# Kernel optimization log

Hardware: AMD Instinct MI355X
Metric: run time of the kernel (lower is better)

The kernel has to match this reference:

```python
import jax, jax.numpy as jnp
import numpy as np
from jax import lax

T_ITERS = 6
LN_EPS = 1e-5

def layer_norm(x, g, b):
    mu = jnp.mean(x, axis=-1, keepdims=True)
    var = jnp.var(x, axis=-1, keepdims=True)
    return (x - mu) * lax.rsqrt(var + LN_EPS) * g + b

def setup_inputs() -> dict:
    key = jax.random.key(0)
    ks = jax.random.split(key, 12)
    B, C_in, S = 8, 128, 33
    hidden = 2 * C_in          # 256
    dim = 256                  # feat_dim
    N = 64
    w = lambda k, shp, s=0.02: (jax.random.normal(k, shp, jnp.float32) * s)
    return {
        "x": jax.random.normal(ks[0], (B, C_in, S, S, S), jnp.float32),
        "templates_init": jax.random.normal(ks[1], (1, N, dim), jnp.float32),
        "conv_w": w(ks[2], (hidden, C_in, 3, 3, 3)),
        "conv_b": jnp.zeros((hidden,), jnp.float32),
        "Wq": w(ks[3], (dim, dim)),
        "Wk": w(ks[4], (hidden, dim)),
        "Wv": w(ks[5], (hidden, dim)),
        "ln_in_g": jnp.ones((hidden,), jnp.float32), "ln_in_b": jnp.zeros((hidden,), jnp.float32),
        "ln_t_g": jnp.ones((dim,), jnp.float32),    "ln_t_b": jnp.zeros((dim,), jnp.float32),
        "ln_m_g": jnp.ones((dim,), jnp.float32),    "ln_m_b": jnp.zeros((dim,), jnp.float32),
        "W1": w(ks[6], (dim, 2 * dim)), "b1": jnp.zeros((2 * dim,), jnp.float32),
        "W2": w(ks[7], (2 * dim, dim)), "b2": jnp.zeros((dim,), jnp.float32),
    }

def reference(x, templates_init, conv_w, conv_b, Wq, Wk, Wv,
              ln_in_g, ln_in_b, ln_t_g, ln_t_b, ln_m_g, ln_m_b,
              W1, b1, W2, b2):
    # project: Conv3d stride 2, no padding, + ReLU
    h = lax.conv_general_dilated(x, conv_w, window_strides=(2, 2, 2),
                                 padding='VALID',
                                 dimension_numbers=('NCDHW', 'OIDHW', 'NCDHW'))
    h = jax.nn.relu(h + conv_b[None, :, None, None, None])
    B, C, X, Y, Z = h.shape
    dim = templates_init.shape[-1]
    N = templates_init.shape[1]
    scale = dim ** (-0.5)
    tokens = h.reshape(B, C, X * Y * Z).transpose(0, 2, 1)   # (B, L, hidden)
    tokens = layer_norm(tokens, ln_in_g, ln_in_b)
    k = tokens @ Wk                                           # (B, L, dim)
    v = tokens @ Wv                                           # (B, L, dim)
    templates = jnp.broadcast_to(templates_init, (B, N, dim))
    attn = None
    for _ in range(T_ITERS):
        t_prev = templates
        t = layer_norm(templates, ln_t_g, ln_t_b)
        q = (t @ Wq) * scale                                  # (B, N, dim)
        attn_logits = jnp.einsum('bnd,bld->bln', q, k)        # (B, L, N)
        attn = jax.nn.softmax(attn_logits, axis=-1)           # competitive over N
        attn = attn + 1e-8
        attn = attn / jnp.sum(attn, axis=-2, keepdims=True)   # renormalize over L
        templates = t_prev + jnp.einsum('bld,bln->bnd', v, attn)
        m = layer_norm(templates, ln_m_g, ln_m_b)
        templates = templates + (jax.nn.gelu(m @ W1 + b1, approximate=False) @ W2 + b2)
    templates_out = templates.transpose(0, 2, 1)              # (B, dim, N)
    attn_out = attn.transpose(0, 2, 1).reshape(B, N, X, Y, Z)
    return templates_out, attn_out
```

## Files before the change

### kernel.cpp

```cpp
#include <hip/hip_runtime.h>

typedef unsigned short u16;
typedef short s16x8 __attribute__((ext_vector_type(8)));
typedef float f32x4 __attribute__((ext_vector_type(4)));
typedef float f32x4u __attribute__((ext_vector_type(4), aligned(4)));
typedef unsigned short us4 __attribute__((ext_vector_type(4)));

__device__ __forceinline__ float bf2f(u16 v) {
    return __uint_as_float(((unsigned int)v) << 16);
}
__device__ __forceinline__ u16 f2bf(float f) {
    unsigned int u = __float_as_uint(f);
    u = u + 0x7FFFu + ((u >> 16) & 1u);
    return (u16)(u >> 16);
}
__device__ __forceinline__ f32x4 mfma16(s16x8 a, s16x8 b, f32x4 c) {
    return __builtin_amdgcn_mfma_f32_16x16x32_bf16(a, b, c, 0, 0, 0);
}
#define ZERO4 f32x4{0.f, 0.f, 0.f, 0.f}

__global__ void prepack_kernel(const float* __restrict__ conv_w, const float* __restrict__ Wk,
                               const float* __restrict__ Wv, const float* __restrict__ Wq,
                               const float* __restrict__ W1, const float* __restrict__ W2,
                               u16* __restrict__ Bp, u16* __restrict__ WkvP, u16* __restrict__ WqP,
                               u16* __restrict__ W1T, u16* __restrict__ W2T)
{
    int idx = blockIdx.x * 256 + threadIdx.x;
    if (idx < 294912) {
        int n = idx / 1152, g = idx - n * 1152;
        int ic = g / 9, r = g - ic * 9;
        const float* s = conv_w + n * 3456 + ic * 27 + r * 3;
        u16* d = Bp + n * 4608 + g * 4;
        d[0] = f2bf(s[0]); d[1] = f2bf(s[1]); d[2] = f2bf(s[2]); d[3] = 0;
    } else if (idx < 425984) {
        int i = idx - 294912;
        int n = i >> 8, c = i & 255;
        WkvP[i] = f2bf((n < 256) ? Wk[c * 256 + n] : Wv[c * 256 + (n - 256)]);
    } else if (idx < 491520) {
        int i = idx - 425984;
        int n = i >> 8, c = i & 255;
        WqP[i] = f2bf(Wq[c * 256 + n]);
    } else if (idx < 622592) {
        int i = idx - 491520;
        int h = i >> 8, c = i & 255;
        W1T[i] = f2bf(W1[c * 512 + h]);
    } else if (idx < 753664) {
        int i = idx - 622592;
        int dd = i >> 9, h = i & 511;
        W2T[i] = f2bf(W2[h * 256 + dd]);
    }
}

__global__ __launch_bounds__(512, 4) void conv_fused(
    const float* __restrict__ x, const u16* __restrict__ Bp, const float* __restrict__ conv_b,
    const float* __restrict__ ln_g, const float* __restrict__ ln_b, const u16* __restrict__ WkvP,
    u16* __restrict__ kbuf, u16* __restrict__ vT)
{
    __shared__ __align__(16) char smem[66816];
    u16* slab0  = (u16*)smem;
    u16* slab1  = (u16*)(smem + 31104);
    u16* tokbf  = (u16*)smem;
    float* lnred  = (float*)(smem + 62208);
    float* lnstat = (float*)(smem + 66304);

    int blk = blockIdx.x;
    int b = blk & 7, ox = (blk >> 5) & 15, oyb = (blk >> 3) & 3;
    int tid = threadIdx.x, wid = tid >> 6, lane = tid & 63;
    int quad = lane >> 4, l15 = lane & 15;
    int nbase = wid * 32;

    f32x4 acc[4][2];
    #pragma unroll
    for (int i = 0; i < 4; ++i)
        #pragma unroll
        for (int j = 0; j < 2; ++j) acc[i][j] = ZERO4;

    const u16* bprow0 = Bp + (nbase + l15) * 4608 + quad * 8;
    const u16* bprow1 = bprow0 + 16 * 4608;

    const float* xp[8]; int so8[8]; unsigned wmask = 0;
    #pragma unroll
    for (int u = 0; u < 8; ++u) {
        int s = tid + u * 512;
        so8[u] = -1; xp[u] = x;
        if (s < 3888) {
            int row = s / 9;
            int c = s - row * 9;
            int icl = row / 27;
            int rr = row - icl * 27;
            int ixl = rr / 9;
            int iyl = rr - ixl * 9;
            const float* xr = x + ((size_t)((b * 128 + icl) * 33) + (2 * ox + ixl)) * 1089
                              + (8 * oyb + iyl) * 33;
            if (c < 8) { xp[u] = xr + c * 4; wmask |= (1u << u); }
            else       { xp[u] = xr + 32; }
            so8[u] = row * 36 + c * 4;
        }
    }
    const size_t ICST = 16ull * 35937;

    f32x4u tv[8];
#define LOADX(ICC)                                                          \
    {                                                                       \
        _Pragma("unroll")                                                   \
        for (int u = 0; u < 8; ++u) {                                       \
            if (so8[u] >= 0) {                                              \
                const float* p = xp[u] + (size_t)(ICC) * ICST;              \
                if ((wmask >> u) & 1u) tv[u] = *(const f32x4u*)p;           \
                else                   tv[u] = f32x4u{p[0], 0.f, 0.f, 0.f}; \
            }                                                               \
        }                                                                   \
    }
#define STOREX(DST)                                                         \
    {                                                                       \
        _Pragma("unroll")                                                   \
        for (int u = 0; u < 8; ++u) {                                       \
            if (so8[u] >= 0) {                                              \
                us4 w;                                                      \
                w.x = f2bf(tv[u].x); w.y = f2bf(tv[u].y);                   \
                w.z = f2bf(tv[u].z); w.w = f2bf(tv[u].w);                   \
                *(us4*)((DST) + so8[u]) = w;                                \
            }                                                               \
        }                                                                   \
    }

    LOADX(0)
    STOREX(slab0)
    __syncthreads();

    for (int icc = 0; icc < 8; ++icc) {
        const u16* cur = (icc & 1) ? slab1 : slab0;
        u16* nxt = (icc & 1) ? slab0 : slab1;
        if (icc < 7) LOADX(icc + 1)

        const u16* bk0 = bprow0 + icc * 576;
        const u16* bk1 = bprow1 + icc * 576;
        s16x8 bbA[2], bbB[2];
        bbA[0] = *reinterpret_cast<const s16x8*>(bk0);
        bbA[1] = *reinterpret_cast<const s16x8*>(bk1);

#define CONV_STEP(CC, BREG)                                                     \
        {                                                                       \
            int g = (CC) * 8 + quad * 2;                                        \
            int i0 = g / 9, r9 = g - i0 * 9;                                    \
            int kx = r9 / 3, ky = r9 - kx * 3;                                  \
            int base0 = (i0 * 27 + kx * 9 + ky) * 36 + 2 * l15;                 \
            g += 1;                                                             \
            i0 = g / 9; r9 = g - i0 * 9; kx = r9 / 3; ky = r9 - kx * 3;         \
            int base1 = (i0 * 27 + kx * 9 + ky) * 36 + 2 * l15;                 \
            _Pragma("unroll")                                                   \
            for (int fm = 0; fm < 4; ++fm) {                                    \
                union { s16x8 v; ushort2 h[4]; } af;                            \
                const u16* sp0 = cur + base0 + fm * 72;                         \
                const u16* sp1 = cur + base1 + fm * 72;                         \
                af.h[0] = *(const ushort2*)(sp0);                               \
                af.h[1] = *(const ushort2*)(sp0 + 2);                           \
                af.h[2] = *(const ushort2*)(sp1);                               \
                af.h[3] = *(const ushort2*)(sp1 + 2);                           \
                acc[fm][0] = mfma16(af.v, (BREG)[0], acc[fm][0]);               \
                acc[fm][1] = mfma16(af.v, (BREG)[1], acc[fm][1]);               \
            }                                                                   \
        }

        #pragma unroll 1
        for (int c8 = 0; c8 < 18; c8 += 2) {
            bbB[0] = *reinterpret_cast<const s16x8*>(bk0 + (c8 + 1) * 32);
            bbB[1] = *reinterpret_cast<const s16x8*>(bk1 + (c8 + 1) * 32);
            CONV_STEP(c8, bbA)
            if (c8 + 2 < 18) {
                bbA[0] = *reinterpret_cast<const s16x8*>(bk0 + (c8 + 2) * 32);
                bbA[1] = *reinterpret_cast<const s16x8*>(bk1 + (c8 + 2) * 32);
            }
            CONV_STEP(c8 + 1, bbB)
        }
#undef CONV_STEP
        if (icc < 7) STOREX(nxt)
        __syncthreads();
    }
#undef LOADX
#undef STOREX

    #pragma unroll
    for (int fn = 0; fn < 2; ++fn) {
        float bias = conv_b[nbase + fn * 16 + l15];
        #pragma unroll
        for (int fm = 0; fm < 4; ++fm)
            #pragma unroll
            for (int r = 0; r < 4; ++r)
                acc[fm][fn][r] = fmaxf(acc[fm][fn][r] + bias, 0.f);
    }
    #pragma unroll
    for (int fm = 0; fm < 4; ++fm) {
        #pragma unroll
        for (int r = 0; r < 4; ++r) {
            float s = acc[fm][0][r] + acc[fm][1][r];
            float q2 = acc[fm][0][r] * acc[fm][0][r] + acc[fm][1][r] * acc[fm][1][r];
            #pragma unroll
            for (int msk = 1; msk <= 8; msk <<= 1) {
                s  += __shfl_xor(s, msk, 64);
                q2 += __shfl_xor(q2, msk, 64);
            }
            if (l15 == 0) {
                int mm = fm * 16 + quad * 4 + r;
                lnred[(wid * 64 + mm) * 2 + 0] = s;
                lnred[(wid * 64 + mm) * 2 + 1] = q2;
            }
        }
    }
    __syncthreads();
    if (tid < 64) {
        float s = 0, q2 = 0;
        #pragma unroll
        for (int w = 0; w < 8; ++w) { s += lnred[(w * 64 + tid) * 2]; q2 += lnred[(w * 64 + tid) * 2 + 1]; }
        float mu = s * (1.f / 256.f);
        float var = fmaxf(q2 * (1.f / 256.f) - mu * mu, 0.f);
        lnstat[tid * 2]     = mu;
        lnstat[tid * 2 + 1] = rsqrtf(var + 1e-5f);
    }
    __syncthreads();
    {
        float gam[2], bet[2];
        #pragma unroll
        for (int fn = 0; fn < 2; ++fn) {
            int n = nbase + fn * 16 + l15;
            gam[fn] = ln_g[n]; bet[fn] = ln_b[n];
        }
        #pragma unroll
        for (int fm = 0; fm < 4; ++fm)
            #pragma unroll
            for (int r = 0; r < 4; ++r) {
                int mm = fm * 16 + quad * 4 + r;
                float mu = lnstat[mm * 2], rs = lnstat[mm * 2 + 1];
                #pragma unroll
                for (int fn = 0; fn < 2; ++fn) {
                    int n = nbase + fn * 16 + l15;
                    tokbf[mm * 264 + n] = f2bf((acc[fm][fn][r] - mu) * rs * gam[fn] + bet[fn]);
                }
            }
    }
    __syncthreads();
    f32x4 kacc[4][4];
    #pragma unroll
    for (int i = 0; i < 4; ++i)
        #pragma unroll
        for (int j = 0; j < 4; ++j) kacc[i][j] = ZERO4;
    int n2 = wid * 64;
    const u16* wp = WkvP + (n2 + l15) * 256 + quad * 8;
    s16x8 wvA[4], wvB[4];
    #pragma unroll
    for (int fn = 0; fn < 4; ++fn) wvA[fn] = *reinterpret_cast<const s16x8*>(wp + fn * 4096);

#define KV_STEP(KK, WREG)                                                           \
    {                                                                               \
        s16x8 a2[4];                                                                \
        _Pragma("unroll")                                                           \
        for (int fm = 0; fm < 4; ++fm)                                              \
            a2[fm] = *reinterpret_cast<const s16x8*>(tokbf + (fm * 16 + l15) * 264  \
                                                     + (KK) * 32 + quad * 8);       \
        _Pragma("unroll")                                                           \
        for (int fn = 0; fn < 4; ++fn)                                              \
            _Pragma("unroll")                                                       \
            for (int fm = 0; fm < 4; ++fm)                                          \
                kacc[fm][fn] = mfma16(a2[fm], (WREG)[fn], kacc[fm][fn]);            \
    }

    #pragma unroll 1
    for (int kc = 0; kc < 8; kc += 2) {
        #pragma unroll
        for (int fn = 0; fn < 4; ++fn)
            wvB[fn] = *reinterpret_cast<const s16x8*>(wp + fn * 4096 + (kc + 1) * 32);
        KV_STEP(kc, wvA)
        if (kc + 2 < 8) {
            #pragma unroll
            for (int fn = 0; fn < 4; ++fn)
                wvA[fn] = *reinterpret_cast<const s16x8*>(wp + fn * 4096 + (kc + 2) * 32);
        }
        KV_STEP(kc + 1, wvB)
    }
#undef KV_STEP

    #pragma unroll
    for (int fm = 0; fm < 4; ++fm)
        #pragma unroll
        for (int r = 0; r < 4; ++r) {
            int l = (ox * 16 + oyb * 4 + fm) * 16 + quad * 4 + r;
            #pragma unroll
            for (int fn = 0; fn < 4; ++fn) {
                int n = n2 + fn * 16 + l15;
                u16 v = f2bf(kacc[fm][fn][r]);
                if (n < 256) kbuf[((b << 12) + l) * 256 + n] = v;
                else         vT[((b * 256 + (n - 256)) << 12) + l] = v;
            }
        }
}

__global__ __launch_bounds__(256) void kQ(
    const float* __restrict__ tinit, float* __restrict__ tpl,
    const float* __restrict__ ln_t_g, const float* __restrict__ ln_t_b,
    const u16* __restrict__ WqP, u16* __restrict__ qbuf, float* __restrict__ delta)
{
    __shared__ __align__(16) u16 mls[64 * 264];
    __shared__ float pls[64][4][2];
    __shared__ float stat[64][2];
    int b = blockIdx.x, tid = threadIdx.x;
    int m = tid >> 2, part = tid & 3;
    const float* tp = tinit + m * 256 + part * 64;
    float* tg = tpl + (b * 64 + m) * 256 + part * 64;
    float s = 0, q2 = 0;
    for (int i = 0; i < 64; ++i) {
        float v = tp[i];
        tg[i] = v;
        s += v; q2 += v * v;
    }
    pls[m][part][0] = s; pls[m][part][1] = q2;
    __syncthreads();
    if (tid < 64) {
        float ss = 0, qq = 0;
        #pragma unroll
        for (int p = 0; p < 4; ++p) { ss += pls[tid][p][0]; qq += pls[tid][p][1]; }
        float mu = ss * (1.f / 256.f);
        float var = fmaxf(qq * (1.f / 256.f) - mu * mu, 0.f);
        stat[tid][0] = mu; stat[tid][1] = rsqrtf(var + 1e-5f);
    }
    __syncthreads();
    {
        float mu = stat[m][0], rs = stat[m][1];
        for (int i = 0; i < 64; ++i) {
            int d = part * 64 + i;
            mls[m * 264 + d] = f2bf((tp[i] - mu) * rs * ln_t_g[d] + ln_t_b[d]);
        }
    }
    __syncthreads();
    int wid = tid >> 6, lane = tid & 63, quad = lane >> 4, l15 = lane & 15;
    f32x4 qa[4][4];
    #pragma unroll
    for (int i = 0; i < 4; ++i)
        #pragma unroll
        for (int j = 0; j < 4; ++j) qa[i][j] = ZERO4;
    #pragma unroll 1
    for (int kc = 0; kc < 8; ++kc) {
        s16x8 a[4];
        #pragma unroll
        for (int fm = 0; fm < 4; ++fm)
            a[fm] = *reinterpret_cast<const s16x8*>(mls + (fm * 16 + l15) * 264 + kc * 32 + quad * 8);
        #pragma unroll
        for (int fn = 0; fn < 4; ++fn) {
            s16x8 bv = *reinterpret_cast<const s16x8*>(WqP + (wid * 64 + fn * 16 + l15) * 256 + kc * 32 + quad * 8);
            #pragma unroll
            for (int fm = 0; fm < 4; ++fm)
                qa[fm][fn] = mfma16(a[fm], bv, qa[fm][fn]);
        }
    }
    #pragma unroll
    for (int fm = 0; fm < 4; ++fm)
        #pragma unroll
        for (int fn = 0; fn < 4; ++fn)
            #pragma unroll
            for (int r = 0; r < 4; ++r) {
                int mt = fm * 16 + quad * 4 + r;
                int d = wid * 64 + fn * 16 + l15;
                qbuf[(b * 64 + mt) * 256 + d] = f2bf(qa[fm][fn][r] * 0.0625f);
            }
    f32x4* dz = (f32x4*)(delta + b * 16384);
    for (int i = tid; i < 4096; i += 256) dz[i] = ZERO4;
}

__global__ __launch_bounds__(512, 2) void kA(
    const u16* __restrict__ qbuf, const u16* __restrict__ kbuf, const u16* __restrict__ vT,
    float* __restrict__ cs_part, float* __restrict__ delta, int last, u16* __restrict__ attnT)
{
    __shared__ __align__(16) u16 qls[64 * 264];
    __shared__ __align__(16) u16 atile[64 * 136];
    __shared__ float colsh[8][64];
    int b = blockIdx.x & 7, ltg = blockIdx.x >> 3;
    int tid = threadIdx.x, wid = tid >> 6, lane = tid & 63;
    int quad = lane >> 4, l15 = lane & 15;

    {
        int r = tid >> 3, c = (tid & 7) * 32;
        const u16* src = qbuf + b * 16384 + r * 256 + c;
        u16* dst = qls + r * 264 + c;
        #pragma unroll
        for (int j = 0; j < 4; ++j)
            *(int4*)(dst + j * 8) = *(const int4*)(src + j * 8);
    }
    int lrow = ltg * 128 + wid * 16;
    const u16* arow = kbuf + (size_t)((b << 12) + lrow + l15) * 256;
    s16x8 av[8];
    #pragma unroll
    for (int kc = 0; kc < 8; ++kc)
        av[kc] = *reinterpret_cast<const s16x8*>(arow + kc * 32 + quad * 8);
    const u16* vrow = vT + ((size_t)(b * 256 + wid * 32 + l15) << 12) + ltg * 128 + quad * 8;
    s16x8 bv2[2][4];
    #pragma unroll
    for (int fn = 0; fn < 2; ++fn)
        #pragma unroll
        for (int kc = 0; kc < 4; ++kc)
            bv2[fn][kc] = *reinterpret_cast<const s16x8*>(vrow + (fn << 16) + kc * 32);
    __syncthreads();
    f32x4 sa[4];
    #pragma unroll
    for (int fn = 0; fn < 4; ++fn) sa[fn] = ZERO4;
    #pragma unroll
    for (int kc = 0; kc < 8; ++kc) {
        #pragma unroll
        for (int fn = 0; fn < 4; ++fn) {
            s16x8 bv = *reinterpret_cast<const s16x8*>(qls + (fn * 16 + l15) * 264 + kc * 32 + quad * 8);
            sa[fn] = mfma16(av[kc], bv, sa[fn]);
        }
    }
    float colp[4] = {0.f, 0.f, 0.f, 0.f};
    #pragma unroll
    for (int r = 0; r < 4; ++r) {
        float mx = fmaxf(fmaxf(sa[0][r], sa[1][r]), fmaxf(sa[2][r], sa[3][r]));
        #pragma unroll
        for (int msk = 1; msk <= 8; msk <<= 1) mx = fmaxf(mx, __shfl_xor(mx, msk, 64));
        float e[4], sum = 0;
        #pragma unroll
        for (int fn = 0; fn < 4; ++fn) { e[fn] = __expf(sa[fn][r] - mx); sum += e[fn]; }
        #pragma unroll
        for (int msk = 1; msk <= 8; msk <<= 1) sum += __shfl_xor(sum, msk, 64);
        float inv = 1.f / sum;
        #pragma unroll
        for (int fn = 0; fn < 4; ++fn) {
            float p = e[fn] * inv + 1e-8f;
            colp[fn] += p;
            atile[(fn * 16 + l15) * 136 + wid * 16 + quad * 4 + r] = f2bf(p);
        }
    }
    #pragma unroll
    for (int fn = 0; fn < 4; ++fn) {
        float c = colp[fn];
        c += __shfl_xor(c, 16, 64);
        c += __shfl_xor(c, 32, 64);
        if (lane < 16) colsh[wid][fn * 16 + lane] = c;
    }
    __syncthreads();
    if (tid < 64) {
        float s = 0;
        #pragma unroll
        for (int w = 0; w < 8; ++w) s += colsh[w][tid];
        cs_part[((b << 5) + ltg) * 64 + tid] = s;
    }
    {
        f32x4 pacc[4][2];
        #pragma unroll
        for (int i = 0; i < 4; ++i)
            #pragma unroll
            for (int j = 0; j < 2; ++j) pacc[i][j] = ZERO4;
        #pragma unroll
        for (int kc = 0; kc < 4; ++kc) {
            #pragma unroll
            for (int fm = 0; fm < 4; ++fm) {
                s16x8 a = *reinterpret_cast<const s16x8*>(atile + (fm * 16 + l15) * 136 + kc * 32 + quad * 8);
                #pragma unroll
                for (int fn = 0; fn < 2; ++fn)
                    pacc[fm][fn] = mfma16(a, bv2[fn][kc], pacc[fm][fn]);
            }
        }
        #pragma unroll
        for (int fm = 0; fm < 4; ++fm)
            #pragma unroll
            for (int fn = 0; fn < 2; ++fn)
                #pragma unroll
                for (int r = 0; r < 4; ++r) {
                    int n = fm * 16 + quad * 4 + r;
                    int d = wid * 32 + fn * 16 + l15;
                    atomicAdd(&delta[(size_t)(b * 64 + n) * 256 + d], pacc[fm][fn][r]);
                }
    }
    if (last) {
        int n = tid >> 3, lo = (tid & 7) * 16;
        const u16* src = atile + n * 136 + lo;
        u16* dst = attnT + (size_t)((b * 64 + n) << 12) + ltg * 128 + lo;
        *(int4*)(dst)     = *(const int4*)(src);
        *(int4*)(dst + 8) = *(const int4*)(src + 8);
    }
}

__global__ __launch_bounds__(512) void kT(
    float* __restrict__ tpl, float* __restrict__ delta, const float* __restrict__ cs_part,
    float* __restrict__ colsum,
    const float* __restrict__ ln_m_g, const float* __restrict__ ln_m_b,
    const u16* __restrict__ W1T, const float* __restrict__ b1,
    const u16* __restrict__ W2T, const float* __restrict__ b2,
    const float* __restrict__ ln_t_g, const float* __restrict__ ln_t_b,
    const u16* __restrict__ WqP, u16* __restrict__ qbuf,
    int last, float* __restrict__ out0)
{
    __shared__ __align__(16) u16 mls[16 * 264];
    __shared__ __align__(16) u16 hid[16 * 520];
    __shared__ float pls[16][32][2];
    __shared__ float stat[16][2];
    __shared__ float lnr2[8][16][2];
    __shared__ float csh[16];
    int b = blockIdx.x & 7, mg = blockIdx.x >> 3;
    int m0 = mg * 16;
    int tid = threadIdx.x, wid = tid >> 6, lane = tid & 63;
    int quad = lane >> 4, l15 = lane & 15;
    if (tid < 16) {
        float s = 0;
        #pragma unroll
        for (int g = 0; g < 32; ++g) s += cs_part[((b << 5) + g) * 64 + m0 + tid];
        csh[tid] = 1.f / s;
        if (last) colsum[b * 64 + m0 + tid] = s;
    }
    __syncthreads();
    {
        int ml = tid >> 5, part = tid & 31;
        float cinv = csh[ml];
        float* tg = tpl + (b * 64 + m0 + ml) * 256 + part * 8;
        float* dg = delta + (size_t)(b * 64 + m0 + ml) * 256 + part * 8;
        float vbuf[8];
        float s = 0, q2 = 0;
        #pragma unroll
        for (int i = 0; i < 8; ++i) {
            float v = tg[i] + dg[i] * cinv;
            vbuf[i] = v; s += v; q2 += v * v;
        }
        if (!last) {
            f32x4* dz = (f32x4*)dg;
            dz[0] = ZERO4; dz[1] = ZERO4;
        }
        pls[ml][part][0] = s; pls[ml][part][1] = q2;
        __syncthreads();
        if (tid < 16) {
            float ss = 0, qq = 0;
            #pragma unroll
            for (int p = 0; p < 32; ++p) { ss += pls[tid][p][0]; qq += pls[tid][p][1]; }
            float mu = ss * (1.f / 256.f);
            float var = fmaxf(qq * (1.f / 256.f) - mu * mu, 0.f);
            stat[tid][0] = mu; stat[tid][1] = rsqrtf(var + 1e-5f);
        }
        __syncthreads();
        float mu = stat[ml][0], rs = stat[ml][1];
        #pragma unroll
        for (int i = 0; i < 8; ++i) {
            int d = part * 8 + i;
            tg[i] = vbuf[i];
            mls[ml * 264 + d] = f2bf((vbuf[i] - mu) * rs * ln_m_g[d] + ln_m_b[d]);
        }
    }
    __syncthreads();
    {
        f32x4 ha[4];
        #pragma unroll
        for (int j = 0; j < 4; ++j) ha[j] = ZERO4;
        #pragma unroll 1
        for (int kc = 0; kc < 8; ++kc) {
            s16x8 a = *reinterpret_cast<const s16x8*>(mls + l15 * 264 + kc * 32 + quad * 8);
            #pragma unroll
            for (int fn = 0; fn < 4; ++fn) {
                s16x8 bv = *reinterpret_cast<const s16x8*>(W1T + (wid * 64 + fn * 16 + l15) * 256 + kc * 32 + quad * 8);
                ha[fn] = mfma16(a, bv, ha[fn]);
            }
        }
        #pragma unroll
        for (int fn = 0; fn < 4; ++fn) {
            int nh = wid * 64 + fn * 16 + l15;
            float bb = b1[nh];
            #pragma unroll
            for (int r = 0; r < 4; ++r) {
                float v = ha[fn][r] + bb;
                v = 0.5f * v * (1.f + erff(v * 0.70710678118654752f));
                hid[(quad * 4 + r) * 520 + nh] = f2bf(v);
            }
        }
    }
    __syncthreads();
    {
        f32x4 oa[2];
        oa[0] = ZERO4; oa[1] = ZERO4;
        #pragma unroll 1
        for (int kc = 0; kc < 16; ++kc) {
            s16x8 a = *reinterpret_cast<const s16x8*>(hid + l15 * 520 + kc * 32 + quad * 8);
            #pragma unroll
            for (int fn = 0; fn < 2; ++fn) {
                s16x8 bv = *reinterpret_cast<const s16x8*>(W2T + (wid * 32 + fn * 16 + l15) * 512 + kc * 32 + quad * 8);
                oa[fn] = mfma16(a, bv, oa[fn]);
            }
        }
        #pragma unroll
        for (int fn = 0; fn < 2; ++fn) {
            int d = wid * 32 + fn * 16 + l15;
            float bb = b2[d];
            #pragma unroll
            for (int r = 0; r < 4; ++r) {
                int mm = quad * 4 + r;
                oa[fn][r] += bb + tpl[(b * 64 + m0 + mm) * 256 + d];
            }
        }
        #pragma unroll
        for (int r = 0; r < 4; ++r) {
            float s = oa[0][r] + oa[1][r];
            float q2 = oa[0][r] * oa[0][r] + oa[1][r] * oa[1][r];
            #pragma unroll
            for (int msk = 1; msk <= 8; msk <<= 1) {
                s  += __shfl_xor(s, msk, 64);
                q2 += __shfl_xor(q2, msk, 64);
            }
            if (l15 == 0) {
                lnr2[wid][quad * 4 + r][0] = s;
                lnr2[wid][quad * 4 + r][1] = q2;
            }
        }
        __syncthreads();
        if (tid < 16) {
            float ss = 0, qq = 0;
            #pragma unroll
            for (int w = 0; w < 8; ++w) { ss += lnr2[w][tid][0]; qq += lnr2[w][tid][1]; }
            float mu = ss * (1.f / 256.f);
            float var = fmaxf(qq * (1.f / 256.f) - mu * mu, 0.f);
            stat[tid][0] = mu; stat[tid][1] = rsqrtf(var + 1e-5f);
        }
        __syncthreads();
        #pragma unroll
        for (int fn = 0; fn < 2; ++fn) {
            int d = wid * 32 + fn * 16 + l15;
            float gg = last ? 0.f : ln_t_g[d];
            float bt = last ? 0.f : ln_t_b[d];
            #pragma unroll
            for (int r = 0; r < 4; ++r) {
                int mm = quad * 4 + r;
                float v = oa[fn][r];
                tpl[(b * 64 + m0 + mm) * 256 + d] = v;
                if (last) {
                    out0[(b * 256 + d) * 64 + m0 + mm] = v;
                } else {
                    mls[mm * 264 + d] = f2bf((v - stat[mm][0]) * stat[mm][1] * gg + bt);
                }
            }
        }
    }
    if (!last) {
        __syncthreads();
        f32x4 qa[2];
        qa[0] = ZERO4; qa[1] = ZERO4;
        #pragma unroll 1
        for (int kc = 0; kc < 8; ++kc) {
            s16x8 a = *reinterpret_cast<const s16x8*>(mls + l15 * 264 + kc * 32 + quad * 8);
            #pragma unroll
            for (int fn = 0; fn < 2; ++fn) {
                s16x8 bv = *reinterpret_cast<const s16x8*>(WqP + (wid * 32 + fn * 16 + l15) * 256 + kc * 32 + quad * 8);
                qa[fn] = mfma16(a, bv, qa[fn]);
            }
        }
        #pragma unroll
        for (int fn = 0; fn < 2; ++fn)
            #pragma unroll
            for (int r = 0; r < 4; ++r) {
                int mt = m0 + quad * 4 + r;
                int d = wid * 32 + fn * 16 + l15;
                qbuf[(b * 64 + mt) * 256 + d] = f2bf(qa[fn][r] * 0.0625f);
            }
    }
}

__global__ void kE(const u16* __restrict__ attnT, const float* __restrict__ colsum,
                   float* __restrict__ out1)
{
    int blk = blockIdx.x;
    int b = blk & 7, r8 = blk >> 3;
    int e = (b << 18) + (r8 << 10) + threadIdx.x * 4;
    int n = (e >> 12) & 63;
    float ci = 1.f / colsum[b * 64 + n];
    const u16* s = attnT + e;
    f32x4 o;
    o.x = bf2f(s[0]) * ci; o.y = bf2f(s[1]) * ci;
    o.z = bf2f(s[2]) * ci; o.w = bf2f(s[3]) * ci;
    *(f32x4*)(out1 + e) = o;
}

extern "C" void kernel_launch(void* const* d_in, const int* in_sizes, int n_in,
                              void* d_out, int out_size, void* d_ws, size_t ws_size,
                              hipStream_t stream)
{
    const float* x       = (const float*)d_in[0];
    const float* tinit   = (const float*)d_in[1];
    const float* conv_w  = (const float*)d_in[2];
    const float* conv_b  = (const float*)d_in[3];
    const float* Wq      = (const float*)d_in[4];
    const float* Wk      = (const float*)d_in[5];
    const float* Wv      = (const float*)d_in[6];
    const float* ln_in_g = (const float*)d_in[7];
    const float* ln_in_b = (const float*)d_in[8];
    const float* ln_t_g  = (const float*)d_in[9];
    const float* ln_t_b  = (const float*)d_in[10];
    const float* ln_m_g  = (const float*)d_in[11];
    const float* ln_m_b  = (const float*)d_in[12];
    const float* W1      = (const float*)d_in[13];
    const float* b1      = (const float*)d_in[14];
    const float* W2      = (const float*)d_in[15];
    const float* b2      = (const float*)d_in[16];

    char* ws = (char*)d_ws;
    u16* Bp       = (u16*)(ws + 0);
    u16* WkvP     = (u16*)(ws + 2359296);
    u16* WqP      = (u16*)(ws + 2621440);
    u16* W1T      = (u16*)(ws + 2752512);
    u16* W2T      = (u16*)(ws + 3014656);
    u16* kbuf     = (u16*)(ws + 3276800);
    u16* vT       = (u16*)(ws + 20054016);
    u16* qbuf     = (u16*)(ws + 36831232);
    u16* attnT    = (u16*)(ws + 37093376);
    float* colsum = (float*)(ws + 41287680);
    float* tpl    = (float*)(ws + 41289728);
    float* delta  = (float*)(ws + 41814016);
    float* cs_part= (float*)(ws + 42338304);

    float* out0 = (float*)d_out;
    float* out1 = out0 + 131072;

    prepack_kernel<<<2944, 256, 0, stream>>>(conv_w, Wk, Wv, Wq, W1, W2, Bp, WkvP, WqP, W1T, W2T);
    conv_fused<<<512, 512, 0, stream>>>(x, Bp, conv_b, ln_in_g, ln_in_b, WkvP, kbuf, vT);
    kQ<<<8, 256, 0, stream>>>(tinit, tpl, ln_t_g, ln_t_b, WqP, qbuf, delta);
    for (int it = 0; it < 6; ++it) {
        int last = (it == 5) ? 1 : 0;
        kA<<<256, 512, 0, stream>>>(qbuf, kbuf, vT, cs_part, delta, last, attnT);
        kT<<<32, 512, 0, stream>>>(tpl, delta, cs_part, colsum, ln_m_g, ln_m_b, W1T, b1, W2T, b2,
                                   ln_t_g, ln_t_b, WqP, qbuf, last, out0);
    }
    kE<<<2048, 256, 0, stream>>>(attnT, colsum, out1);
}
```

Measured before the change: 716.8 us.

## Fuse the iteration loop into one persistent kernel with atomic-counter grid sync

The six kA/kT launch pairs and the final kE kernel are replaced by a single persistent kernel of 256 blocks. Blocks synchronise per batch through global atomic counters with spin-waits, and a subset of blocks runs the template MLP and Q update while the others wait for the per-batch q-ready flag. The K rows stay in registers across iterations, and the attention output normalisation is folded into the last iteration. This removes about 13 launch gaps and reloads, at the cost of spin-wait serialisation and a risk of deadlock if the 256 blocks are not all co-resident.

```diff
diff --git a/kernel.cpp b/kernel.cpp
--- a/kernel.cpp
+++ b/kernel.cpp
@@ -18,6 +18,21 @@
     return __builtin_amdgcn_mfma_f32_16x16x32_bf16(a, b, c, 0, 0, 0);
 }
 #define ZERO4 f32x4{0.f, 0.f, 0.f, 0.f}
+
+__device__ __forceinline__ void spin_until(unsigned* c, unsigned v) {
+    if (threadIdx.x == 0) {
+        while (__hip_atomic_load(c, __ATOMIC_ACQUIRE, __HIP_MEMORY_SCOPE_AGENT) != v)
+            __builtin_amdgcn_s_sleep(4);
+    }
+    __syncthreads();
+}
+__device__ __forceinline__ void arrive(unsigned* c) {
+    __syncthreads();
+    if (threadIdx.x == 0) {
+        __threadfence();
+        __hip_atomic_fetch_add(c, 1u, __ATOMIC_RELEASE, __HIP_MEMORY_SCOPE_AGENT);
+    }
+}
 
 __global__ void prepack_kernel(const float* __restrict__ conv_w, const float* __restrict__ Wk,
                                const float* __restrict__ Wv, const float* __restrict__ Wq,
@@ -297,12 +312,14 @@
 __global__ __launch_bounds__(256) void kQ(
     const float* __restrict__ tinit, float* __restrict__ tpl,
     const float* __restrict__ ln_t_g, const float* __restrict__ ln_t_b,
-    const u16* __restrict__ WqP, u16* __restrict__ qbuf, float* __restrict__ delta)
+    const u16* __restrict__ WqP, u16* __restrict__ qbuf, float* __restrict__ delta,
+    unsigned* __restrict__ cnts)
 {
     __shared__ __align__(16) u16 mls[64 * 264];
     __shared__ float pls[64][4][2];
     __shared__ float stat[64][2];
     int b = blockIdx.x, tid = threadIdx.x;
+    if (b == 0 && tid < 96) cnts[tid] = 0;
     int m = tid >> 2, part = tid & 3;
     const float* tp = tinit + m * 256 + part * 64;
     float* tg = tpl + (b * 64 + m) * 256 + part * 64;
@@ -365,310 +382,316 @@
     for (int i = tid; i < 4096; i += 256) dz[i] = ZERO4;
 }
 
-__global__ __launch_bounds__(512, 2) void kA(
-    const u16* __restrict__ qbuf, const u16* __restrict__ kbuf, const u16* __restrict__ vT,
-    float* __restrict__ cs_part, float* __restrict__ delta, int last, u16* __restrict__ attnT)
-{
-    __shared__ __align__(16) u16 qls[64 * 264];
-    __shared__ __align__(16) u16 atile[64 * 136];
-    __shared__ float colsh[8][64];
-    int b = blockIdx.x & 7, ltg = blockIdx.x >> 3;
-    int tid = threadIdx.x, wid = tid >> 6, lane = tid & 63;
-    int quad = lane >> 4, l15 = lane & 15;
-
-    {
-        int r = tid >> 3, c = (tid & 7) * 32;
-        const u16* src = qbuf + b * 16384 + r * 256 + c;
-        u16* dst = qls + r * 264 + c;
-        #pragma unroll
-        for (int j = 0; j < 4; ++j)
-            *(int4*)(dst + j * 8) = *(const int4*)(src + j * 8);
-    }
-    int lrow = ltg * 128 + wid * 16;
-    const u16* arow = kbuf + (size_t)((b << 12) + lrow + l15) * 256;
-    s16x8 av[8];
-    #pragma unroll
-    for (int kc = 0; kc < 8; ++kc)
-        av[kc] = *reinterpret_cast<const s16x8*>(arow + kc * 32 + quad * 8);
-    const u16* vrow = vT + ((size_t)(b * 256 + wid * 32 + l15) << 12) + ltg * 128 + quad * 8;
-    s16x8 bv2[2][4];
-    #pragma unroll
-    for (int fn = 0; fn < 2; ++fn)
-        #pragma unroll
-        for (int kc = 0; kc < 4; ++kc)
-            bv2[fn][kc] = *reinterpret_cast<const s16x8*>(vrow + (fn << 16) + kc * 32);
-    __syncthreads();
-    f32x4 sa[4];
-    #pragma unroll
-    for (int fn = 0; fn < 4; ++fn) sa[fn] = ZERO4;
-    #pragma unroll
-    for (int kc = 0; kc < 8; ++kc) {
-        #pragma unroll
-        for (int fn = 0; fn < 4; ++fn) {
-            s16x8 bv = *reinterpret_cast<const s16x8*>(qls + (fn * 16 + l15) * 264 + kc * 32 + quad * 8);
-            sa[fn] = mfma16(av[kc], bv, sa[fn]);
-        }
-    }
-    float colp[4] = {0.f, 0.f, 0.f, 0.f};
-    #pragma unroll
-    for (int r = 0; r < 4; ++r) {
-        float mx = fmaxf(fmaxf(sa[0][r], sa[1][r]), fmaxf(sa[2][r], sa[3][r]));
-        #pragma unroll
-        for (int msk = 1; msk <= 8; msk <<= 1) mx = fmaxf(mx, __shfl_xor(mx, msk, 64));
-        float e[4], sum = 0;
-        #pragma unroll
-        for (int fn = 0; fn < 4; ++fn) { e[fn] = __expf(sa[fn][r] - mx); sum += e[fn]; }
-        #pragma unroll
-        for (int msk = 1; msk <= 8; msk <<= 1) sum += __shfl_xor(sum, msk, 64);
-        float inv = 1.f / sum;
-        #pragma unroll
-        for (int fn = 0; fn < 4; ++fn) {
-            float p = e[fn] * inv + 1e-8f;
-            colp[fn] += p;
-            atile[(fn * 16 + l15) * 136 + wid * 16 + quad * 4 + r] = f2bf(p);
-        }
-    }
-    #pragma unroll
-    for (int fn = 0; fn < 4; ++fn) {
-        float c = colp[fn];
-        c += __shfl_xor(c, 16, 64);
-        c += __shfl_xor(c, 32, 64);
-        if (lane < 16) colsh[wid][fn * 16 + lane] = c;
-    }
-    __syncthreads();
-    if (tid < 64) {
-        float s = 0;
-        #pragma unroll
-        for (int w = 0; w < 8; ++w) s += colsh[w][tid];
-        cs_part[((b << 5) + ltg) * 64 + tid] = s;
-    }
-    {
-        f32x4 pacc[4][2];
-        #pragma unroll
-        for (int i = 0; i < 4; ++i)
-            #pragma unroll
-            for (int j = 0; j < 2; ++j) pacc[i][j] = ZERO4;
-        #pragma unroll
-        for (int kc = 0; kc < 4; ++kc) {
-            #pragma unroll
-            for (int fm = 0; fm < 4; ++fm) {
-                s16x8 a = *reinterpret_cast<const s16x8*>(atile + (fm * 16 + l15) * 136 + kc * 32 + quad * 8);
-                #pragma unroll
-                for (int fn = 0; fn < 2; ++fn)
-                    pacc[fm][fn] = mfma16(a, bv2[fn][kc], pacc[fm][fn]);
-            }
-        }
-        #pragma unroll
-        for (int fm = 0; fm < 4; ++fm)
-            #pragma unroll
-            for (int fn = 0; fn < 2; ++fn)
-                #pragma unroll
-                for (int r = 0; r < 4; ++r) {
-                    int n = fm * 16 + quad * 4 + r;
-                    int d = wid * 32 + fn * 16 + l15;
-                    atomicAdd(&delta[(size_t)(b * 64 + n) * 256 + d], pacc[fm][fn][r]);
-                }
-    }
-    if (last) {
-        int n = tid >> 3, lo = (tid & 7) * 16;
-        const u16* src = atile + n * 136 + lo;
-        u16* dst = attnT + (size_t)((b * 64 + n) << 12) + ltg * 128 + lo;
-        *(int4*)(dst)     = *(const int4*)(src);
-        *(int4*)(dst + 8) = *(const int4*)(src + 8);
-    }
-}
-
-__global__ __launch_bounds__(512) void kT(
-    float* __restrict__ tpl, float* __restrict__ delta, const float* __restrict__ cs_part,
-    float* __restrict__ colsum,
+__global__ __launch_bounds__(512, 2) void kMega(
+    u16* __restrict__ qbuf, const u16* __restrict__ kbuf, const u16* __restrict__ vT,
+    float* __restrict__ cs_part, float* __restrict__ delta, u16* __restrict__ attnT,
+    float* __restrict__ tpl,
     const float* __restrict__ ln_m_g, const float* __restrict__ ln_m_b,
     const u16* __restrict__ W1T, const float* __restrict__ b1,
     const u16* __restrict__ W2T, const float* __restrict__ b2,
     const float* __restrict__ ln_t_g, const float* __restrict__ ln_t_b,
-    const u16* __restrict__ WqP, u16* __restrict__ qbuf,
-    int last, float* __restrict__ out0)
+    const u16* __restrict__ WqP,
+    unsigned* __restrict__ cnt, unsigned* __restrict__ qrdy,
+    float* __restrict__ out0, float* __restrict__ out1)
 {
-    __shared__ __align__(16) u16 mls[16 * 264];
-    __shared__ __align__(16) u16 hid[16 * 520];
-    __shared__ float pls[16][32][2];
-    __shared__ float stat[16][2];
-    __shared__ float lnr2[8][16][2];
-    __shared__ float csh[16];
-    int b = blockIdx.x & 7, mg = blockIdx.x >> 3;
-    int m0 = mg * 16;
+    __shared__ __align__(16) char smem[53248];
+    u16* qls     = (u16*)smem;
+    u16* atile   = (u16*)(smem + 33792);
+    float* colsh = (float*)(smem + 51200);
+    u16* mls    = (u16*)smem;
+    u16* hid    = (u16*)(smem + 8448);
+    float* pls  = (float*)(smem + 25088);
+    float* stat = (float*)(smem + 29184);
+    float* lnr2 = (float*)(smem + 29312);
+    float* csh  = (float*)(smem + 30336);
+
+    int b = blockIdx.x & 7, ltg = blockIdx.x >> 3;
     int tid = threadIdx.x, wid = tid >> 6, lane = tid & 63;
     int quad = lane >> 4, l15 = lane & 15;
-    if (tid < 16) {
-        float s = 0;
-        #pragma unroll
-        for (int g = 0; g < 32; ++g) s += cs_part[((b << 5) + g) * 64 + m0 + tid];
-        csh[tid] = 1.f / s;
-        if (last) colsum[b * 64 + m0 + tid] = s;
-    }
-    __syncthreads();
-    {
-        int ml = tid >> 5, part = tid & 31;
-        float cinv = csh[ml];
-        float* tg = tpl + (b * 64 + m0 + ml) * 256 + part * 8;
-        float* dg = delta + (size_t)(b * 64 + m0 + ml) * 256 + part * 8;
-        float vbuf[8];
-        float s = 0, q2 = 0;
-        #pragma unroll
-        for (int i = 0; i < 8; ++i) {
-            float v = tg[i] + dg[i] * cinv;
-            vbuf[i] = v; s += v; q2 += v * v;
-        }
-        if (!last) {
-            f32x4* dz = (f32x4*)dg;
-            dz[0] = ZERO4; dz[1] = ZERO4;
-        }
-        pls[ml][part][0] = s; pls[ml][part][1] = q2;
+
+    int lrow = ltg * 128 + wid * 16;
+    const u16* arow = kbuf + (size_t)((b << 12) + lrow + l15) * 256;
+    s16x8 av[8];
+    #pragma unroll
+    for (int kc = 0; kc < 8; ++kc)
+        av[kc] = *reinterpret_cast<const s16x8*>(arow + kc * 32 + quad * 8);
+    const u16* vrow = vT + ((size_t)(b * 256 + wid * 32 + l15) << 12) + ltg * 128 + quad * 8;
+
+    #pragma unroll 1
+    for (int it = 0; it < 6; ++it) {
+        int last = (it == 5);
+        if (it > 0) spin_until(&qrdy[b * 6 + it - 1], 4u);
+        {
+            int r = tid >> 3, c = (tid & 7) * 32;
+            const u16* src = qbuf + b * 16384 + r * 256 + c;
+            u16* dst = qls + r * 264 + c;
+            #pragma unroll
+            for (int j = 0; j < 4; ++j)
+                *(int4*)(dst + j * 8) = *(const int4*)(src + j * 8);
+        }
+        s16x8 bv2[2][4];
+        #pragma unroll
+        for (int fn = 0; fn < 2; ++fn)
+            #pragma unroll
+            for (int kc = 0; kc < 4; ++kc)
+                bv2[fn][kc] = *reinterpret_cast<const s16x8*>(vrow + (fn << 16) + kc * 32);
         __syncthreads();
-        if (tid < 16) {
-            float ss = 0, qq = 0;
-            #pragma unroll
-            for (int p = 0; p < 32; ++p) { ss += pls[tid][p][0]; qq += pls[tid][p][1]; }
-            float mu = ss * (1.f / 256.f);
-            float var = fmaxf(qq * (1.f / 256.f) - mu * mu, 0.f);
-            stat[tid][0] = mu; stat[tid][1] = rsqrtf(var + 1e-5f);
+        f32x4 sa[4];
+        #pragma unroll
+        for (int fn = 0; fn < 4; ++fn) sa[fn] = ZERO4;
+        #pragma unroll
+        for (int kc = 0; kc < 8; ++kc) {
+            #pragma unroll
+            for (int fn = 0; fn < 4; ++fn) {
+                s16x8 bv = *reinterpret_cast<const s16x8*>(qls + (fn * 16 + l15) * 264 + kc * 32 + quad * 8);
+                sa[fn] = mfma16(av[kc], bv, sa[fn]);
+            }
+        }
+        float colp[4] = {0.f, 0.f, 0.f, 0.f};
+        #pragma unroll
+        for (int r = 0; r < 4; ++r) {
+            float mx = fmaxf(fmaxf(sa[0][r], sa[1][r]), fmaxf(sa[2][r], sa[3][r]));
+            #pragma unroll
+            for (int msk = 1; msk <= 8; msk <<= 1) mx = fmaxf(mx, __shfl_xor(mx, msk, 64));
+            float e[4], sum = 0;
+            #pragma unroll
+            for (int fn = 0; fn < 4; ++fn) { e[fn] = __expf(sa[fn][r] - mx); sum += e[fn]; }
+            #pragma unroll
+            for (int msk = 1; msk <= 8; msk <<= 1) sum += __shfl_xor(sum, msk, 64);
+            float inv = 1.f / sum;
+            #pragma unroll
+            for (int fn = 0; fn < 4; ++fn) {
+                float p = e[fn] * inv + 1e-8f;
+                colp[fn] += p;
+                atile[(fn * 16 + l15) * 136 + wid * 16 + quad * 4 + r] = f2bf(p);
+            }
+        }
+        #pragma unroll
+        for (int fn = 0; fn < 4; ++fn) {
+            float c = colp[fn];
+            c += __shfl_xor(c, 16, 64);
+            c += __shfl_xor(c, 32, 64);
+            if (lane < 16) colsh[wid * 64 + fn * 16 + lane] = c;
         }
         __syncthreads();
-        float mu = stat[ml][0], rs = stat[ml][1];
-        #pragma unroll
-        for (int i = 0; i < 8; ++i) {
-            int d = part * 8 + i;
-            tg[i] = vbuf[i];
-            mls[ml * 264 + d] = f2bf((vbuf[i] - mu) * rs * ln_m_g[d] + ln_m_b[d]);
-        }
-    }
-    __syncthreads();
-    {
-        f32x4 ha[4];
-        #pragma unroll
-        for (int j = 0; j < 4; ++j) ha[j] = ZERO4;
-        #pragma unroll 1
-        for (int kc = 0; kc < 8; ++kc) {
-            s16x8 a = *reinterpret_cast<const s16x8*>(mls + l15 * 264 + kc * 32 + quad * 8);
-            #pragma unroll
-            for (int fn = 0; fn < 4; ++fn) {
-                s16x8 bv = *reinterpret_cast<const s16x8*>(W1T + (wid * 64 + fn * 16 + l15) * 256 + kc * 32 + quad * 8);
-                ha[fn] = mfma16(a, bv, ha[fn]);
-            }
-        }
-        #pragma unroll
-        for (int fn = 0; fn < 4; ++fn) {
-            int nh = wid * 64 + fn * 16 + l15;
-            float bb = b1[nh];
-            #pragma unroll
-            for (int r = 0; r < 4; ++r) {
-                float v = ha[fn][r] + bb;
-                v = 0.5f * v * (1.f + erff(v * 0.70710678118654752f));
-                hid[(quad * 4 + r) * 520 + nh] = f2bf(v);
-            }
-        }
-    }
-    __syncthreads();
-    {
-        f32x4 oa[2];
-        oa[0] = ZERO4; oa[1] = ZERO4;
-        #pragma unroll 1
-        for (int kc = 0; kc < 16; ++kc) {
-            s16x8 a = *reinterpret_cast<const s16x8*>(hid + l15 * 520 + kc * 32 + quad * 8);
-            #pragma unroll
-            for (int fn = 0; fn < 2; ++fn) {
-                s16x8 bv = *reinterpret_cast<const s16x8*>(W2T + (wid * 32 + fn * 16 + l15) * 512 + kc * 32 + quad * 8);
-                oa[fn] = mfma16(a, bv, oa[fn]);
-            }
-        }
-        #pragma unroll
-        for (int fn = 0; fn < 2; ++fn) {
-            int d = wid * 32 + fn * 16 + l15;
-            float bb = b2[d];
-            #pragma unroll
-            for (int r = 0; r < 4; ++r) {
-                int mm = quad * 4 + r;
-                oa[fn][r] += bb + tpl[(b * 64 + m0 + mm) * 256 + d];
-            }
-        }
-        #pragma unroll
-        for (int r = 0; r < 4; ++r) {
-            float s = oa[0][r] + oa[1][r];
-            float q2 = oa[0][r] * oa[0][r] + oa[1][r] * oa[1][r];
-            #pragma unroll
-            for (int msk = 1; msk <= 8; msk <<= 1) {
-                s  += __shfl_xor(s, msk, 64);
-                q2 += __shfl_xor(q2, msk, 64);
-            }
-            if (l15 == 0) {
-                lnr2[wid][quad * 4 + r][0] = s;
-                lnr2[wid][quad * 4 + r][1] = q2;
-            }
-        }
-        __syncthreads();
-        if (tid < 16) {
-            float ss = 0, qq = 0;
-            #pragma unroll
-            for (int w = 0; w < 8; ++w) { ss += lnr2[w][tid][0]; qq += lnr2[w][tid][1]; }
-            float mu = ss * (1.f / 256.f);
-            float var = fmaxf(qq * (1.f / 256.f) - mu * mu, 0.f);
-            stat[tid][0] = mu; stat[tid][1] = rsqrtf(var + 1e-5f);
-        }
-        __syncthreads();
-        #pragma unroll
-        for (int fn = 0; fn < 2; ++fn) {
-            int d = wid * 32 + fn * 16 + l15;
-            float gg = last ? 0.f : ln_t_g[d];
-            float bt = last ? 0.f : ln_t_b[d];
-            #pragma unroll
-            for (int r = 0; r < 4; ++r) {
-                int mm = quad * 4 + r;
-                float v = oa[fn][r];
-                tpl[(b * 64 + m0 + mm) * 256 + d] = v;
-                if (last) {
-                    out0[(b * 256 + d) * 64 + m0 + mm] = v;
-                } else {
-                    mls[mm * 264 + d] = f2bf((v - stat[mm][0]) * stat[mm][1] * gg + bt);
-                }
-            }
-        }
-    }
-    if (!last) {
-        __syncthreads();
-        f32x4 qa[2];
-        qa[0] = ZERO4; qa[1] = ZERO4;
-        #pragma unroll 1
-        for (int kc = 0; kc < 8; ++kc) {
-            s16x8 a = *reinterpret_cast<const s16x8*>(mls + l15 * 264 + kc * 32 + quad * 8);
-            #pragma unroll
-            for (int fn = 0; fn < 2; ++fn) {
-                s16x8 bv = *reinterpret_cast<const s16x8*>(WqP + (wid * 32 + fn * 16 + l15) * 256 + kc * 32 + quad * 8);
-                qa[fn] = mfma16(a, bv, qa[fn]);
-            }
-        }
-        #pragma unroll
-        for (int fn = 0; fn < 2; ++fn)
-            #pragma unroll
-            for (int r = 0; r < 4; ++r) {
-                int mt = m0 + quad * 4 + r;
-                int d = wid * 32 + fn * 16 + l15;
-                qbuf[(b * 64 + mt) * 256 + d] = f2bf(qa[fn][r] * 0.0625f);
-            }
-    }
-}
-
-__global__ void kE(const u16* __restrict__ attnT, const float* __restrict__ colsum,
-                   float* __restrict__ out1)
-{
-    int blk = blockIdx.x;
-    int b = blk & 7, r8 = blk >> 3;
-    int e = (b << 18) + (r8 << 10) + threadIdx.x * 4;
-    int n = (e >> 12) & 63;
-    float ci = 1.f / colsum[b * 64 + n];
-    const u16* s = attnT + e;
-    f32x4 o;
-    o.x = bf2f(s[0]) * ci; o.y = bf2f(s[1]) * ci;
-    o.z = bf2f(s[2]) * ci; o.w = bf2f(s[3]) * ci;
-    *(f32x4*)(out1 + e) = o;
+        if (tid < 64) {
+            float s = 0;
+            #pragma unroll
+            for (int w = 0; w < 8; ++w) s += colsh[w * 64 + tid];
+            cs_part[((b << 5) + ltg) * 64 + tid] = s;
+        }
+        {
+            f32x4 pacc[4][2];
+            #pragma unroll
+            for (int i = 0; i < 4; ++i)
+                #pragma unroll
+                for (int j = 0; j < 2; ++j) pacc[i][j] = ZERO4;
+            #pragma unroll
+            for (int kc = 0; kc < 4; ++kc) {
+                #pragma unroll
+                for (int fm = 0; fm < 4; ++fm) {
+                    s16x8 a = *reinterpret_cast<const s16x8*>(atile + (fm * 16 + l15) * 136 + kc * 32 + quad * 8);
+                    #pragma unroll
+                    for (int fn = 0; fn < 2; ++fn)
+                        pacc[fm][fn] = mfma16(a, bv2[fn][kc], pacc[fm][fn]);
+                }
+            }
+            #pragma unroll
+            for (int fm = 0; fm < 4; ++fm)
+                #pragma unroll
+                for (int fn = 0; fn < 2; ++fn)
+                    #pragma unroll
+                    for (int r = 0; r < 4; ++r) {
+                        int n = fm * 16 + quad * 4 + r;
+                        int d = wid * 32 + fn * 16 + l15;
+                        atomicAdd(&delta[(size_t)(b * 64 + n) * 256 + d], pacc[fm][fn][r]);
+                    }
+        }
+        if (last) {
+            int n = tid >> 3, lo = (tid & 7) * 16;
+            const u16* src = atile + n * 136 + lo;
+            u16* dst = attnT + (size_t)((b * 64 + n) << 12) + ltg * 128 + lo;
+            *(int4*)(dst)     = *(const int4*)(src);
+            *(int4*)(dst + 8) = *(const int4*)(src + 8);
+        }
+        arrive(&cnt[b * 6 + it]);
+
+        if (ltg < 4) {
+            spin_until(&cnt[b * 6 + it], 32u);
+            int m0 = ltg * 16;
+            if (tid < 16) {
+                float s = 0;
+                #pragma unroll
+                for (int g = 0; g < 32; ++g) s += cs_part[((b << 5) + g) * 64 + m0 + tid];
+                csh[tid] = 1.f / s;
+            }
+            __syncthreads();
+            {
+                int ml = tid >> 5, part = tid & 31;
+                float cinv = csh[ml];
+                float* tg = tpl + (b * 64 + m0 + ml) * 256 + part * 8;
+                float* dg = delta + (size_t)(b * 64 + m0 + ml) * 256 + part * 8;
+                float vbuf[8];
+                float s = 0, q2 = 0;
+                #pragma unroll
+                for (int i = 0; i < 8; ++i) {
+                    float v = tg[i] + dg[i] * cinv;
+                    vbuf[i] = v; s += v; q2 += v * v;
+                }
+                if (!last) {
+                    f32x4* dz = (f32x4*)dg;
+                    dz[0] = ZERO4; dz[1] = ZERO4;
+                }
+                pls[(ml * 32 + part) * 2 + 0] = s; pls[(ml * 32 + part) * 2 + 1] = q2;
+                __syncthreads();
+                if (tid < 16) {
+                    float ss = 0, qq = 0;
+                    #pragma unroll
+                    for (int p = 0; p < 32; ++p) { ss += pls[(tid * 32 + p) * 2]; qq += pls[(tid * 32 + p) * 2 + 1]; }
+                    float mu = ss * (1.f / 256.f);
+                    float var = fmaxf(qq * (1.f / 256.f) - mu * mu, 0.f);
+                    stat[tid * 2] = mu; stat[tid * 2 + 1] = rsqrtf(var + 1e-5f);
+                }
+                __syncthreads();
+                float mu = stat[ml * 2], rs = stat[ml * 2 + 1];
+                #pragma unroll
+                for (int i = 0; i < 8; ++i) {
+                    int d = part * 8 + i;
+                    tg[i] = vbuf[i];
+                    mls[ml * 264 + d] = f2bf((vbuf[i] - mu) * rs * ln_m_g[d] + ln_m_b[d]);
+                }
+            }
+            __syncthreads();
+            {
+                f32x4 ha[4];
+                #pragma unroll
+                for (int j = 0; j < 4; ++j) ha[j] = ZERO4;
+                #pragma unroll 1
+                for (int kc = 0; kc < 8; ++kc) {
+                    s16x8 a = *reinterpret_cast<const s16x8*>(mls + l15 * 264 + kc * 32 + quad * 8);
+                    #pragma unroll
+                    for (int fn = 0; fn < 4; ++fn) {
+                        s16x8 bv = *reinterpret_cast<const s16x8*>(W1T + (wid * 64 + fn * 16 + l15) * 256 + kc * 32 + quad * 8);
+                        ha[fn] = mfma16(a, bv, ha[fn]);
+                    }
+                }
+                #pragma unroll
+                for (int fn = 0; fn < 4; ++fn) {
+                    int nh = wid * 64 + fn * 16 + l15;
+                    float bb = b1[nh];
+                    #pragma unroll
+                    for (int r = 0; r < 4; ++r) {
+                        float v = ha[fn][r] + bb;
+                        v = 0.5f * v * (1.f + erff(v * 0.70710678118654752f));
+                        hid[(quad * 4 + r) * 520 + nh] = f2bf(v);
+                    }
+                }
+            }
+            __syncthreads();
+            {
+                f32x4 oa[2];
+                oa[0] = ZERO4; oa[1] = ZERO4;
+                #pragma unroll 1
+                for (int kc = 0; kc < 16; ++kc) {
+                    s16x8 a = *reinterpret_cast<const s16x8*>(hid + l15 * 520 + kc * 32 + quad * 8);
+                    #pragma unroll
+                    for (int fn = 0; fn < 2; ++fn) {
+                        s16x8 bv = *reinterpret_cast<const s16x8*>(W2T + (wid * 32 + fn * 16 + l15) * 512 + kc * 32 + quad * 8);
+                        oa[fn] = mfma16(a, bv, oa[fn]);
+                    }
+                }
+                #pragma unroll
+                for (int fn = 0; fn < 2; ++fn) {
+                    int d = wid * 32 + fn * 16 + l15;
+                    float bb = b2[d];
+                    #pragma unroll
+                    for (int r = 0; r < 4; ++r) {
+                        int mm = quad * 4 + r;
+                        oa[fn][r] += bb + tpl[(b * 64 + m0 + mm) * 256 + d];
+                    }
+                }
+                #pragma unroll
+                for (int r = 0; r < 4; ++r) {
+                    float s = oa[0][r] + oa[1][r];
+                    float q2 = oa[0][r] * oa[0][r] + oa[1][r] * oa[1][r];
+                    #pragma unroll
+                    for (int msk = 1; msk <= 8; msk <<= 1) {
+                        s  += __shfl_xor(s, msk, 64);
+                        q2 += __shfl_xor(q2, msk, 64);
+                    }
+                    if (l15 == 0) {
+                        lnr2[(wid * 16 + quad * 4 + r) * 2 + 0] = s;
+                        lnr2[(wid * 16 + quad * 4 + r) * 2 + 1] = q2;
+                    }
+                }
+                __syncthreads();
+                if (tid < 16) {
+                    float ss = 0, qq = 0;
+                    #pragma unroll
+                    for (int w = 0; w < 8; ++w) { ss += lnr2[(w * 16 + tid) * 2]; qq += lnr2[(w * 16 + tid) * 2 + 1]; }
+                    float mu = ss * (1.f / 256.f);
+                    float var = fmaxf(qq * (1.f / 256.f) - mu * mu, 0.f);
+                    stat[tid * 2] = mu; stat[tid * 2 + 1] = rsqrtf(var + 1e-5f);
+                }
+                __syncthreads();
+                #pragma unroll
+                for (int fn = 0; fn < 2; ++fn) {
+                    int d = wid * 32 + fn * 16 + l15;
+                    float gg = last ? 0.f : ln_t_g[d];
+                    float bt = last ? 0.f : ln_t_b[d];
+                    #pragma unroll
+                    for (int r = 0; r < 4; ++r) {
+                        int mm = quad * 4 + r;
+                        float v = oa[fn][r];
+                        tpl[(b * 64 + m0 + mm) * 256 + d] = v;
+                        if (last) {
+                            out0[(b * 256 + d) * 64 + m0 + mm] = v;
+                        } else {
+                            mls[mm * 264 + d] = f2bf((v - stat[mm * 2]) * stat[mm * 2 + 1] * gg + bt);
+                        }
+                    }
+                }
+            }
+            if (!last) {
+                __syncthreads();
+                f32x4 qa[2];
+                qa[0] = ZERO4; qa[1] = ZERO4;
+                #pragma unroll 1
+                for (int kc = 0; kc < 8; ++kc) {
+                    s16x8 a = *reinterpret_cast<const s16x8*>(mls + l15 * 264 + kc * 32 + quad * 8);
+                    #pragma unroll
+                    for (int fn = 0; fn < 2; ++fn) {
+                        s16x8 bv = *reinterpret_cast<const s16x8*>(WqP + (wid * 32 + fn * 16 + l15) * 256 + kc * 32 + quad * 8);
+                        qa[fn] = mfma16(a, bv, qa[fn]);
+                    }
+                }
+                #pragma unroll
+                for (int fn = 0; fn < 2; ++fn)
+                    #pragma unroll
+                    for (int r = 0; r < 4; ++r) {
+                        int mt = m0 + quad * 4 + r;
+                        int d = wid * 32 + fn * 16 + l15;
+                        qbuf[(b * 64 + mt) * 256 + d] = f2bf(qa[fn][r] * 0.0625f);
+                    }
+                arrive(&qrdy[b * 6 + it]);
+            } else {
+                __syncthreads();
+                int n = m0 + (tid >> 5);
+                int c0 = (tid & 31) * 128;
+                float ci = csh[tid >> 5];
+                const u16* src = attnT + ((size_t)(b * 64 + n) << 12) + c0;
+                float* dst = out1 + ((size_t)(b * 64 + n) << 12) + c0;
+                #pragma unroll
+                for (int j = 0; j < 128; j += 4) {
+                    us4 w = *(const us4*)(src + j);
+                    f32x4 o;
+                    o.x = bf2f(w.x) * ci; o.y = bf2f(w.y) * ci;
+                    o.z = bf2f(w.z) * ci; o.w = bf2f(w.w) * ci;
+                    *(f32x4*)(dst + j) = o;
+                }
+            }
+        }
+    }
 }
 
 extern "C" void kernel_launch(void* const* d_in, const int* in_sizes, int n_in,
@@ -703,7 +726,7 @@
     u16* vT       = (u16*)(ws + 20054016);
     u16* qbuf     = (u16*)(ws + 36831232);
     u16* attnT    = (u16*)(ws + 37093376);
-    float* colsum = (float*)(ws + 41287680);
+    unsigned* cnts= (unsigned*)(ws + 41287680);
     float* tpl    = (float*)(ws + 41289728);
     float* delta  = (float*)(ws + 41814016);
     float* cs_part= (float*)(ws + 42338304);
@@ -711,14 +734,13 @@
     float* out0 = (float*)d_out;
     float* out1 = out0 + 131072;
 
+    unsigned* cnt  = cnts;
+    unsigned* qrdy = cnts + 48;
+
     prepack_kernel<<<2944, 256, 0, stream>>>(conv_w, Wk, Wv, Wq, W1, W2, Bp, WkvP, WqP, W1T, W2T);
     conv_fused<<<512, 512, 0, stream>>>(x, Bp, conv_b, ln_in_g, ln_in_b, WkvP, kbuf, vT);
-    kQ<<<8, 256, 0, stream>>>(tinit, tpl, ln_t_g, ln_t_b, WqP, qbuf, delta);
-    for (int it = 0; it < 6; ++it) {
-        int last = (it == 5) ? 1 : 0;
-        kA<<<256, 512, 0, stream>>>(qbuf, kbuf, vT, cs_part, delta, last, attnT);
-        kT<<<32, 512, 0, stream>>>(tpl, delta, cs_part, colsum, ln_m_g, ln_m_b, W1T, b1, W2T, b2,
-                                   ln_t_g, ln_t_b, WqP, qbuf, last, out0);
-    }
-    kE<<<2048, 256, 0, stream>>>(attnT, colsum, out1);
-}
+    kQ<<<8, 256, 0, stream>>>(tinit, tpl, ln_t_g, ln_t_b, WqP, qbuf, delta, cnts);
+    kMega<<<256, 512, 0, stream>>>(qbuf, kbuf, vT, cs_part, delta, attnT, tpl,
+                                   ln_m_g, ln_m_b, W1T, b1, W2T, b2,
+                                   ln_t_g, ln_t_b, WqP, cnt, qrdy, out0, out1);
+}
```

New measurement: 1.463 ms. 104% more time.
